# Optimization experiments

Hardware: AMD Instinct MI355X
Metric: run time of the kernel (lower is better)

Reference implementation:

```python
import jax, jax.numpy as jnp
import numpy as np

B, T, E, HEAD_S = 8, 4096, 2048, 128


def setup_inputs() -> dict:
    key = jax.random.key(0)
    kx, kq, kk, kv = jax.random.split(key, 4)
    x = jax.random.normal(kx, (B, T, E), dtype=jnp.float32)
    # Linear weights initialized ~N(0, 0.02) as in the repo's _init_weights
    Wq = jax.random.normal(kq, (E, HEAD_S), dtype=jnp.float32) * 0.02
    Wk = jax.random.normal(kk, (E, HEAD_S), dtype=jnp.float32) * 0.02
    Wv = jax.random.normal(kv, (E, HEAD_S), dtype=jnp.float32) * 0.02
    return {"x": x, "Wq": Wq, "Wk": Wk, "Wv": Wv}


def reference(x, Wq, Wk, Wv):
    # x: [B,T,E]; W*: [E,D]
    q = jnp.einsum('bte,ed->btd', x, Wq)
    k = jnp.einsum('bte,ed->btd', x, Wk)
    v = jnp.einsum('bte,ed->btd', x, Wv)
    scale = k.shape[-1] ** -0.5
    # scores: [B, T(query), S(key)]
    wei = jnp.einsum('btd,bsd->bts', q, k) * scale
    Tn = x.shape[1]
    causal = jnp.tril(jnp.ones((Tn, Tn), dtype=bool))  # [T,S], True where allowed
    wei = jnp.where(causal[None, :, :], wei, -jnp.inf)
    # NOTE: original code applies softmax over dim=1 (the QUERY axis) —
    # faithful reproduction of that behavior. Each key-column j has finite
    # entries for queries i >= j, so no NaNs arise.
    wei = jax.nn.softmax(wei, axis=1)
    # dropout is identity in eval mode
    out = jnp.einsum('bts,bsd->btd', wei, v)  # [B,T,D]
    return out
```

## Files before the change

kernel.cpp:

```cpp
#include <hip/hip_runtime.h>
#include <hip/hip_bf16.h>

#define TLEN 4096
#define EDIM 2048
#define DDIM 128
#define BSZ  8
#define NT   32
#define MROWS (BSZ*TLEN)
#define NSLOT 528

typedef unsigned short u16;
typedef __attribute__((ext_vector_type(8))) short bf16x8;
typedef __attribute__((ext_vector_type(4))) float f32x4;

#define C1F (0.08838834764831845f * 1.4426950408889634f)

__device__ __forceinline__ u16 f2bf(float f) {
  unsigned u = __builtin_bit_cast(unsigned, f);
  u += 0x7FFFu + ((u >> 16) & 1u);
  return (u16)(u >> 16);
}
__device__ __forceinline__ float bf2f(u16 h) {
  unsigned u = ((unsigned)h) << 16;
  return __builtin_bit_cast(float, u);
}

__device__ __forceinline__ void async_ld16(const void* g, void* lds) {
  __builtin_amdgcn_global_load_lds(
      (const __attribute__((address_space(1))) unsigned int*)(g),
      (__attribute__((address_space(3))) unsigned int*)(lds), 16, 0, 0);
}

__device__ __forceinline__ int swz16(int row, int chunk) {
  return row * 256 + ((chunk ^ (row & 15)) << 4);
}
__device__ __forceinline__ int swz8(int row, int chunk) {
  return row * 128 + ((chunk ^ (row & 7)) << 4);
}

__global__ __launch_bounds__(256) void zero_f32(float* __restrict__ out,
                                                float* __restrict__ denom) {
  size_t i = (size_t)blockIdx.x * 256 + threadIdx.x;
  float4 z = {0.f, 0.f, 0.f, 0.f};
  if (i < (size_t)MROWS * DDIM / 4) ((float4*)out)[i] = z;
  if (i < (size_t)BSZ * TLEN / 4) ((float4*)denom)[i] = z;
}

__global__ __launch_bounds__(256) void prep_w(const float* __restrict__ Wq,
                                              const float* __restrict__ Wk,
                                              const float* __restrict__ Wv,
                                              u16* __restrict__ Wt) {
  int g = blockIdx.x * 256 + threadIdx.x;
  int w = g >> 15;
  int rem = g & 32767;
  int n = rem >> 8;
  int k0 = (rem & 255) * 8;
  const float* W = (w == 0) ? Wq : (w == 1) ? Wk : Wv;
  unsigned pk[4];
  for (int i = 0; i < 4; ++i) {
    u16 lo = f2bf(W[(size_t)(k0 + 2 * i) * DDIM + n]);
    u16 hi = f2bf(W[(size_t)(k0 + 2 * i + 1) * DDIM + n]);
    pk[i] = (unsigned)lo | ((unsigned)hi << 16);
  }
  uint4 v; v.x = pk[0]; v.y = pk[1]; v.z = pk[2]; v.w = pk[3];
  *(uint4*)(Wt + ((size_t)(w * DDIM + n) * EDIM + k0)) = v;
}

__global__ __launch_bounds__(512, 2) void qkv_gemm(const float* __restrict__ x,
                                                   const u16* __restrict__ Wt,
                                                   u16* __restrict__ qkvb) {
  __shared__ u16 As[128 * 64];
  __shared__ u16 Bs[384 * 64];
  const int tid = threadIdx.x, lane = tid & 63, wave = tid >> 6;
  const int quad = lane >> 4, l15 = lane & 15;
  const int m0 = blockIdx.x * 128;
  const int wm = wave & 1, wn = wave >> 1;

  const f32x4 zero = {0.f, 0.f, 0.f, 0.f};
  f32x4 acc[4][6];
  for (int mi = 0; mi < 4; ++mi)
    for (int ni = 0; ni < 6; ++ni) acc[mi][ni] = zero;

  int arow[4], af4[4];
  for (int i = 0; i < 4; ++i) {
    int c = i * 512 + tid;
    arow[i] = c >> 4;
    af4[i] = c & 15;
  }
  float4 ap[4];
#define LOADA(KT)                                                            \
  for (int i = 0; i < 4; ++i)                                                \
    ap[i] = *(const float4*)(x + (size_t)(m0 + arow[i]) * EDIM + (KT)*64 +   \
                             af4[i] * 4);
  LOADA(0)

  for (int kt = 0; kt < EDIM / 64; ++kt) {
    __syncthreads();
    for (int i = 0; i < 4; ++i) {
      uint2 pk;
      pk.x = (unsigned)f2bf(ap[i].x) | ((unsigned)f2bf(ap[i].y) << 16);
      pk.y = (unsigned)f2bf(ap[i].z) | ((unsigned)f2bf(ap[i].w) << 16);
      *(uint2*)((char*)As + swz8(arow[i], af4[i] >> 1) + (af4[i] & 1) * 8) = pk;
    }
    {
      const int k0 = kt * 64;
      for (int e = 0; e < 6; ++e) {
        int rb = (wave * 6 + e) * 8;
        int r = rb + (lane >> 3);
        int c = (lane & 7) ^ (r & 7);
        async_ld16((const char*)(Wt + (size_t)r * EDIM + k0) + c * 16,
                   (char*)Bs + rb * 128);
      }
    }
    __builtin_amdgcn_s_waitcnt(0);
    __syncthreads();
    if (kt + 1 < EDIM / 64) { LOADA(kt + 1) }
    for (int ks = 0; ks < 2; ++ks) {
      const int ch = ks * 4 + quad;
      bf16x8 afr[4], bfr[6];
      for (int mi = 0; mi < 4; ++mi)
        afr[mi] = *(const bf16x8*)((char*)As + swz8(wm * 64 + mi * 16 + l15, ch));
      for (int ni = 0; ni < 6; ++ni)
        bfr[ni] = *(const bf16x8*)((char*)Bs + swz8(wn * 96 + ni * 16 + l15, ch));
      for (int mi = 0; mi < 4; ++mi)
        for (int ni = 0; ni < 6; ++ni)
          acc[mi][ni] = __builtin_amdgcn_mfma_f32_16x16x32_bf16(afr[mi], bfr[ni], acc[mi][ni], 0, 0, 0);
    }
  }
#undef LOADA
  for (int mi = 0; mi < 4; ++mi)
    for (int ni = 0; ni < 6; ++ni) {
      int n = wn * 96 + ni * 16 + l15;
      u16* ob = qkvb + (size_t)(n >> 7) * MROWS * DDIM;
      int nc = n & 127;
      for (int r = 0; r < 4; ++r) {
        int row = m0 + wm * 64 + mi * 16 + quad * 4 + r;
        ob[(size_t)row * DDIM + nc] = f2bf(acc[mi][ni][r]);
      }
    }
}

__global__ __launch_bounds__(256) void score_k(const u16* __restrict__ qb,
                                               const u16* __restrict__ kb,
                                               char* __restrict__ Epack,
                                               float* __restrict__ denom) {
  __shared__ u16 Kbuf[128 * 128];
  __shared__ u16 Qbuf[128 * 128];
  const int tid = threadIdx.x, lane = tid & 63, wave = tid >> 6;
  const int quad = lane >> 4, l15 = lane & 15;
  const int jt = blockIdx.x, ic = blockIdx.y, b = blockIdx.z;
  const int len = NT - jt;
  const int cl = (len + 3) >> 2;
  if (ic * cl >= len) return;
  const int beg = jt + ic * cl;
  const int end = (beg + cl < NT) ? beg + cl : NT;
  const int j0 = jt * 128;

  {
    const char* gk = (const char*)kb + (size_t)(b * TLEN + j0) * 256;
    for (int e = 0; e < 8; ++e) {
      int rb = (wave * 8 + e) * 4;
      int r = rb + (lane >> 4);
      int c = l15 ^ (r & 15);
      async_ld16(gk + r * 256 + c * 16, (char*)Kbuf + rb * 256);
    }
  }
  __builtin_amdgcn_s_waitcnt(0);
  __syncthreads();

  float csum[8];
  for (int ni = 0; ni < 8; ++ni) csum[ni] = 0.f;
  const f32x4 zero = {0.f, 0.f, 0.f, 0.f};

  for (int it = beg; it < end; ++it) {
    const int i0 = it * 128;
    {
      const char* gq = (const char*)qb + (size_t)(b * TLEN + i0) * 256;
      for (int e = 0; e < 8; ++e) {
        int rb = (wave * 8 + e) * 4;
        int r = rb + (lane >> 4);
        int c = l15 ^ (r & 15);
        async_ld16(gq + r * 256 + c * 16, (char*)Qbuf + rb * 256);
      }
    }
    __builtin_amdgcn_s_waitcnt(0);

    f32x4 accS[2][8];
    for (int mi = 0; mi < 2; ++mi)
      for (int ni = 0; ni < 8; ++ni) accS[mi][ni] = zero;
    for (int ks = 0; ks < 4; ++ks) {
      const int ch = ks * 4 + quad;
      bf16x8 afr[2], kfr[8];
      for (int mi = 0; mi < 2; ++mi)
        afr[mi] = *(const bf16x8*)((char*)Qbuf + swz16(wave * 32 + mi * 16 + l15, ch));
      for (int ni = 0; ni < 8; ++ni)
        kfr[ni] = *(const bf16x8*)((char*)Kbuf + swz16(ni * 16 + l15, ch));
      for (int mi = 0; mi < 2; ++mi)
        for (int ni = 0; ni < 8; ++ni)
          accS[mi][ni] = __builtin_amdgcn_mfma_f32_16x16x32_bf16(afr[mi], kfr[ni], accS[mi][ni], 0, 0, 0);
    }
    const bool diag = (it == jt);
    for (int mi = 0; mi < 2; ++mi)
      for (int ni = 0; ni < 8; ++ni)
        for (int r = 0; r < 4; ++r) {
          float e = exp2f(C1F * accS[mi][ni][r]);
          int rrow = wave * 32 + mi * 16 + quad * 4 + r;
          int jl = ni * 16 + l15;
          if (diag && (i0 + rrow) < (j0 + jl)) e = 0.f;
          csum[ni] += e;
          *(u16*)((char*)Qbuf + swz16(rrow, jl >> 3) + (jl & 7) * 2) = f2bf(e);
        }
    char* eslot = Epack + (((size_t)b * NSLOT + (size_t)it * (it + 1) / 2 + jt) << 15);
    for (int e = 0; e < 8; ++e) {
      int row = wave * 32 + e * 4 + (lane >> 4);
      bf16x8 v = *(const bf16x8*)((char*)Qbuf + swz16(row, l15));
      *(bf16x8*)(eslot + row * 256 + l15 * 16) = v;
    }
  }
  for (int ni = 0; ni < 8; ++ni) {
    csum[ni] += __shfl_xor(csum[ni], 16, 64);
    csum[ni] += __shfl_xor(csum[ni], 32, 64);
  }
  __syncthreads();
  float* red = (float*)Kbuf;
  if (lane < 16)
    for (int ni = 0; ni < 8; ++ni)
      red[wave * 128 + ni * 16 + lane] = csum[ni];
  __syncthreads();
  if (tid < 128)
    atomicAdd(&denom[(size_t)b * TLEN + j0 + tid],
              red[tid] + red[128 + tid] + red[256 + tid] + red[384 + tid]);
}

__global__ __launch_bounds__(256) void vscale_t(const u16* __restrict__ vb,
                                                const float* __restrict__ denom,
                                                u16* __restrict__ vbT) {
  __shared__ u16 tile[128 * 136];
  const int tid = threadIdx.x;
  const int t0 = blockIdx.x * 128, b = blockIdx.y;
  for (int i = 0; i < 8; ++i) {
    int c = tid + i * 256;
    int tl = c >> 4, ch = c & 15;
    float rd = 1.0f / denom[(size_t)b * TLEN + t0 + tl];
    uint4 v = *(const uint4*)(vb + ((size_t)(b * TLEN + t0 + tl) * DDIM + ch * 8));
    unsigned w[4] = {v.x, v.y, v.z, v.w};
    unsigned o[4];
    for (int j = 0; j < 4; ++j) {
      float lo = bf2f((u16)w[j]) * rd;
      float hi = bf2f((u16)(w[j] >> 16)) * rd;
      o[j] = (unsigned)f2bf(lo) | ((unsigned)f2bf(hi) << 16);
    }
    uint4 ov; ov.x = o[0]; ov.y = o[1]; ov.z = o[2]; ov.w = o[3];
    *(uint4*)(tile + tl * 136 + ch * 8) = ov;
  }
  __syncthreads();
  for (int i = 0; i < 8; ++i) {
    int c = tid + i * 256;
    int d = c >> 4, ch = c & 15;
    unsigned pk[4];
    for (int j = 0; j < 4; ++j) {
      u16 lo = tile[(ch * 8 + 2 * j) * 136 + d];
      u16 hi = tile[(ch * 8 + 2 * j + 1) * 136 + d];
      pk[j] = (unsigned)lo | ((unsigned)hi << 16);
    }
    uint4 v; v.x = pk[0]; v.y = pk[1]; v.z = pk[2]; v.w = pk[3];
    *(uint4*)(vbT + ((size_t)(b * DDIM + d) * TLEN + t0 + ch * 8)) = v;
  }
}

__global__ __launch_bounds__(256, 3) void pv_k(const char* __restrict__ Epack,
                                               const u16* __restrict__ vbT,
                                               float* __restrict__ out) {
  __shared__ u16 Es[128 * 64];
  __shared__ u16 Vs[128 * 64];
  const int tid = threadIdx.x, lane = tid & 63, wave = tid >> 6;
  const int quad = lane >> 4, l15 = lane & 15;
  const int it = blockIdx.x, jc = blockIdx.y, b = blockIdx.z;
  const int nsub = 2 * (it + 1);
  const int sBeg = jc * 16;
  if (sBeg >= nsub) return;
  const int sEnd = (sBeg + 16 < nsub) ? sBeg + 16 : nsub;
  const int i0 = it * 128;
  const int wm = wave & 1, wn = wave >> 1;

  const f32x4 zero = {0.f, 0.f, 0.f, 0.f};
  f32x4 accO[4][4];
  for (int mi = 0; mi < 4; ++mi)
    for (int ni = 0; ni < 4; ++ni) accO[mi][ni] = zero;

  const size_t triBase = ((size_t)b * NSLOT + (size_t)it * (it + 1) / 2) << 15;
  const char* vbase = (const char*)vbT + (size_t)b * DDIM * TLEN * 2;

  for (int s = sBeg; s < sEnd; ++s) {
    const int jt = s >> 1, h = s & 1;
    __syncthreads();
    {
      const char* eb = Epack + triBase + ((size_t)jt << 15) + h * 128;
      const char* vb2 = vbase + s * 128;
      for (int e = 0; e < 4; ++e) {
        int rb = (wave * 4 + e) * 8;
        int r = rb + (lane >> 3);
        int c = (lane & 7) ^ (r & 7);
        async_ld16(eb + r * 256 + c * 16, (char*)Es + rb * 128);
        async_ld16(vb2 + (size_t)r * (TLEN * 2) + c * 16, (char*)Vs + rb * 128);
      }
    }
    __builtin_amdgcn_s_waitcnt(0);
    __syncthreads();
    for (int ks = 0; ks < 2; ++ks) {
      const int ch = ks * 4 + quad;
      bf16x8 afr[4], bfr[4];
      for (int mi = 0; mi < 4; ++mi)
        afr[mi] = *(const bf16x8*)((char*)Es + swz8(wm * 64 + mi * 16 + l15, ch));
      for (int ni = 0; ni < 4; ++ni)
        bfr[ni] = *(const bf16x8*)((char*)Vs + swz8(wn * 64 + ni * 16 + l15, ch));
      for (int mi = 0; mi < 4; ++mi)
        for (int ni = 0; ni < 4; ++ni)
          accO[mi][ni] = __builtin_amdgcn_mfma_f32_16x16x32_bf16(afr[mi], bfr[ni], accO[mi][ni], 0, 0, 0);
    }
  }
  const bool excl = (it < 8);
  for (int mi = 0; mi < 4; ++mi)
    for (int ni = 0; ni < 4; ++ni) {
      int d = wn * 64 + ni * 16 + l15;
      for (int r = 0; r < 4; ++r) {
        int row = i0 + wm * 64 + mi * 16 + quad * 4 + r;
        float* dst = &out[((size_t)b * TLEN + row) * DDIM + d];
        if (excl) *dst = accO[mi][ni][r];
        else atomicAdd(dst, accO[mi][ni][r]);
      }
    }
}

extern "C" void kernel_launch(void* const* d_in, const int* in_sizes, int n_in,
                              void* d_out, int out_size, void* d_ws, size_t ws_size,
                              hipStream_t stream) {
  const float* x  = (const float*)d_in[0];
  const float* Wq = (const float*)d_in[1];
  const float* Wk = (const float*)d_in[2];
  const float* Wv = (const float*)d_in[3];
  float* out = (float*)d_out;

  u16* qb  = (u16*)d_ws;
  u16* kb  = qb  + (size_t)MROWS * DDIM;
  u16* vb  = kb  + (size_t)MROWS * DDIM;
  u16* vbT = vb  + (size_t)MROWS * DDIM;
  u16* Wt  = vbT + (size_t)MROWS * DDIM;
  float* denom = (float*)(Wt + (size_t)3 * DDIM * EDIM);
  char* Epack = (char*)(denom + (size_t)BSZ * TLEN);

  hipLaunchKernelGGL(zero_f32, dim3(4096), dim3(256), 0, stream, out, denom);
  hipLaunchKernelGGL(prep_w, dim3(384), dim3(256), 0, stream, Wq, Wk, Wv, Wt);
  hipLaunchKernelGGL(qkv_gemm, dim3(256), dim3(512), 0, stream, x, Wt, qb);
  hipLaunchKernelGGL(score_k, dim3(NT, 4, BSZ), dim3(256), 0, stream, qb, kb, Epack, denom);
  hipLaunchKernelGGL(vscale_t, dim3(NT, BSZ), dim3(256), 0, stream, vb, denom, vbT);
  hipLaunchKernelGGL(pv_k, dim3(NT, 4, BSZ), dim3(256), 0, stream, Epack, vbT, out);
}
```

Measured before the change: 623.5 us.

## Drop LDS staging in score and PV kernels, load operands directly from global

score_k now swaps operand roles (K as A, Q as B) so the exponentials can be packed and written straight to the E slab without an LDS transpose, and reads Q fragments directly from global memory instead of staging them in shared memory. The column-sum reduction moves to 16-lane shuffles. pv_k drops its LDS tiles and barriers, reads E and V fragments directly from global, walks full 128-wide key tiles, reverses block order so the largest rows start first, and halves the key split (excl threshold adjusted). Launch bounds also change for qkv_gemm and score_k. The trade is fewer barriers and LDS traffic against uncoalesced or repeated global loads that rely on cache hits.

```diff
diff --git a/kernel.cpp b/kernel.cpp
--- a/kernel.cpp
+++ b/kernel.cpp
@@ -66,7 +66,7 @@
   *(uint4*)(Wt + ((size_t)(w * DDIM + n) * EDIM + k0)) = v;
 }
 
-__global__ __launch_bounds__(512, 2) void qkv_gemm(const float* __restrict__ x,
+__global__ __launch_bounds__(512, 1) void qkv_gemm(const float* __restrict__ x,
                                                    const u16* __restrict__ Wt,
                                                    u16* __restrict__ qkvb) {
   __shared__ u16 As[128 * 64];
@@ -140,12 +140,12 @@
     }
 }
 
-__global__ __launch_bounds__(256) void score_k(const u16* __restrict__ qb,
-                                               const u16* __restrict__ kb,
-                                               char* __restrict__ Epack,
-                                               float* __restrict__ denom) {
+__global__ __launch_bounds__(256, 2) void score_k(const u16* __restrict__ qb,
+                                                  const u16* __restrict__ kb,
+                                                  char* __restrict__ Epack,
+                                                  float* __restrict__ denom) {
   __shared__ u16 Kbuf[128 * 128];
-  __shared__ u16 Qbuf[128 * 128];
+  __shared__ float red[512];
   const int tid = threadIdx.x, lane = tid & 63, wave = tid >> 6;
   const int quad = lane >> 4, l15 = lane & 15;
   const int jt = blockIdx.x, ic = blockIdx.y, b = blockIdx.z;
@@ -157,7 +157,7 @@
   const int j0 = jt * 128;
 
   {
-    const char* gk = (const char*)kb + (size_t)(b * TLEN + j0) * 256;
+    const char* gk = (const char*)kb + ((size_t)b * TLEN + j0) * 256;
     for (int e = 0; e < 8; ++e) {
       int rb = (wave * 8 + e) * 4;
       int r = rb + (lane >> 4);
@@ -168,64 +168,62 @@
   __builtin_amdgcn_s_waitcnt(0);
   __syncthreads();
 
-  float csum[8];
-  for (int ni = 0; ni < 8; ++ni) csum[ni] = 0.f;
+  float csum[8][4];
+  for (int mi = 0; mi < 8; ++mi)
+    for (int r = 0; r < 4; ++r) csum[mi][r] = 0.f;
   const f32x4 zero = {0.f, 0.f, 0.f, 0.f};
+  const char* qtile0 = (const char*)qb + (size_t)b * TLEN * 256;
 
   for (int it = beg; it < end; ++it) {
     const int i0 = it * 128;
-    {
-      const char* gq = (const char*)qb + (size_t)(b * TLEN + i0) * 256;
-      for (int e = 0; e < 8; ++e) {
-        int rb = (wave * 8 + e) * 4;
-        int r = rb + (lane >> 4);
-        int c = l15 ^ (r & 15);
-        async_ld16(gq + r * 256 + c * 16, (char*)Qbuf + rb * 256);
-      }
-    }
-    __builtin_amdgcn_s_waitcnt(0);
-
-    f32x4 accS[2][8];
-    for (int mi = 0; mi < 2; ++mi)
-      for (int ni = 0; ni < 8; ++ni) accS[mi][ni] = zero;
+    const char* gq = qtile0 + (size_t)i0 * 256;
+    f32x4 acc[8][2];
+    for (int mi = 0; mi < 8; ++mi)
+      for (int ni = 0; ni < 2; ++ni) acc[mi][ni] = zero;
     for (int ks = 0; ks < 4; ++ks) {
       const int ch = ks * 4 + quad;
-      bf16x8 afr[2], kfr[8];
-      for (int mi = 0; mi < 2; ++mi)
-        afr[mi] = *(const bf16x8*)((char*)Qbuf + swz16(wave * 32 + mi * 16 + l15, ch));
-      for (int ni = 0; ni < 8; ++ni)
-        kfr[ni] = *(const bf16x8*)((char*)Kbuf + swz16(ni * 16 + l15, ch));
-      for (int mi = 0; mi < 2; ++mi)
-        for (int ni = 0; ni < 8; ++ni)
-          accS[mi][ni] = __builtin_amdgcn_mfma_f32_16x16x32_bf16(afr[mi], kfr[ni], accS[mi][ni], 0, 0, 0);
+      bf16x8 kfr[8], qfr[2];
+      for (int ni = 0; ni < 2; ++ni)
+        qfr[ni] = *(const bf16x8*)(gq + (size_t)(wave * 32 + ni * 16 + l15) * 256 + ch * 16);
+      for (int mi = 0; mi < 8; ++mi)
+        kfr[mi] = *(const bf16x8*)((char*)Kbuf + swz16(mi * 16 + l15, ch));
+      for (int mi = 0; mi < 8; ++mi)
+        for (int ni = 0; ni < 2; ++ni)
+          acc[mi][ni] = __builtin_amdgcn_mfma_f32_16x16x32_bf16(kfr[mi], qfr[ni], acc[mi][ni], 0, 0, 0);
     }
     const bool diag = (it == jt);
-    for (int mi = 0; mi < 2; ++mi)
-      for (int ni = 0; ni < 8; ++ni)
+    char* eslot = Epack + (((size_t)b * NSLOT + (size_t)it * (it + 1) / 2 + jt) << 15);
+    for (int mi = 0; mi < 8; ++mi) {
+      const int jbase = mi * 16 + quad * 4;
+      for (int ni = 0; ni < 2; ++ni) {
+        const int il = wave * 32 + ni * 16 + l15;
+        float ev[4];
         for (int r = 0; r < 4; ++r) {
-          float e = exp2f(C1F * accS[mi][ni][r]);
-          int rrow = wave * 32 + mi * 16 + quad * 4 + r;
-          int jl = ni * 16 + l15;
-          if (diag && (i0 + rrow) < (j0 + jl)) e = 0.f;
-          csum[ni] += e;
-          *(u16*)((char*)Qbuf + swz16(rrow, jl >> 3) + (jl & 7) * 2) = f2bf(e);
+          float e = __builtin_amdgcn_exp2f(C1F * acc[mi][ni][r]);
+          if (diag && (i0 + il) < (j0 + jbase + r)) e = 0.f;
+          csum[mi][r] += e;
+          ev[r] = e;
         }
-    char* eslot = Epack + (((size_t)b * NSLOT + (size_t)it * (it + 1) / 2 + jt) << 15);
-    for (int e = 0; e < 8; ++e) {
-      int row = wave * 32 + e * 4 + (lane >> 4);
-      bf16x8 v = *(const bf16x8*)((char*)Qbuf + swz16(row, l15));
-      *(bf16x8*)(eslot + row * 256 + l15 * 16) = v;
-    }
-  }
-  for (int ni = 0; ni < 8; ++ni) {
-    csum[ni] += __shfl_xor(csum[ni], 16, 64);
-    csum[ni] += __shfl_xor(csum[ni], 32, 64);
-  }
-  __syncthreads();
-  float* red = (float*)Kbuf;
-  if (lane < 16)
-    for (int ni = 0; ni < 8; ++ni)
-      red[wave * 128 + ni * 16 + lane] = csum[ni];
+        uint2 pk;
+        pk.x = (unsigned)f2bf(ev[0]) | ((unsigned)f2bf(ev[1]) << 16);
+        pk.y = (unsigned)f2bf(ev[2]) | ((unsigned)f2bf(ev[3]) << 16);
+        *(uint2*)(eslot + (size_t)il * 256 + jbase * 2) = pk;
+      }
+    }
+  }
+  for (int mi = 0; mi < 8; ++mi)
+    for (int r = 0; r < 4; ++r) {
+      float v = csum[mi][r];
+      v += __shfl_xor(v, 1, 64);
+      v += __shfl_xor(v, 2, 64);
+      v += __shfl_xor(v, 4, 64);
+      v += __shfl_xor(v, 8, 64);
+      csum[mi][r] = v;
+    }
+  if (l15 == 0)
+    for (int mi = 0; mi < 8; ++mi)
+      for (int r = 0; r < 4; ++r)
+        red[wave * 128 + mi * 16 + quad * 4 + r] = csum[mi][r];
   __syncthreads();
   if (tid < 128)
     atomicAdd(&denom[(size_t)b * TLEN + j0 + tid],
@@ -271,15 +269,12 @@
 __global__ __launch_bounds__(256, 3) void pv_k(const char* __restrict__ Epack,
                                                const u16* __restrict__ vbT,
                                                float* __restrict__ out) {
-  __shared__ u16 Es[128 * 64];
-  __shared__ u16 Vs[128 * 64];
   const int tid = threadIdx.x, lane = tid & 63, wave = tid >> 6;
   const int quad = lane >> 4, l15 = lane & 15;
-  const int it = blockIdx.x, jc = blockIdx.y, b = blockIdx.z;
-  const int nsub = 2 * (it + 1);
-  const int sBeg = jc * 16;
-  if (sBeg >= nsub) return;
-  const int sEnd = (sBeg + 16 < nsub) ? sBeg + 16 : nsub;
+  const int it = NT - 1 - blockIdx.x, jc = blockIdx.y, b = blockIdx.z;
+  const int jtBeg = jc * 16;
+  if (jtBeg > it) return;
+  const int jtEnd = (jtBeg + 16 < it + 1) ? jtBeg + 16 : it + 1;
   const int i0 = it * 128;
   const int wm = wave & 1, wn = wave >> 1;
 
@@ -288,38 +283,25 @@
   for (int mi = 0; mi < 4; ++mi)
     for (int ni = 0; ni < 4; ++ni) accO[mi][ni] = zero;
 
-  const size_t triBase = ((size_t)b * NSLOT + (size_t)it * (it + 1) / 2) << 15;
+  const char* triBase = Epack + (((size_t)b * NSLOT + (size_t)it * (it + 1) / 2) << 15);
   const char* vbase = (const char*)vbT + (size_t)b * DDIM * TLEN * 2;
 
-  for (int s = sBeg; s < sEnd; ++s) {
-    const int jt = s >> 1, h = s & 1;
-    __syncthreads();
-    {
-      const char* eb = Epack + triBase + ((size_t)jt << 15) + h * 128;
-      const char* vb2 = vbase + s * 128;
-      for (int e = 0; e < 4; ++e) {
-        int rb = (wave * 4 + e) * 8;
-        int r = rb + (lane >> 3);
-        int c = (lane & 7) ^ (r & 7);
-        async_ld16(eb + r * 256 + c * 16, (char*)Es + rb * 128);
-        async_ld16(vb2 + (size_t)r * (TLEN * 2) + c * 16, (char*)Vs + rb * 128);
-      }
-    }
-    __builtin_amdgcn_s_waitcnt(0);
-    __syncthreads();
-    for (int ks = 0; ks < 2; ++ks) {
-      const int ch = ks * 4 + quad;
+  for (int jt = jtBeg; jt < jtEnd; ++jt) {
+    const char* eb = triBase + ((size_t)jt << 15);
+    const char* vb2 = vbase + jt * 256;
+    for (int ks = 0; ks < 4; ++ks) {
+      const int choff = (ks * 4 + quad) * 16;
       bf16x8 afr[4], bfr[4];
       for (int mi = 0; mi < 4; ++mi)
-        afr[mi] = *(const bf16x8*)((char*)Es + swz8(wm * 64 + mi * 16 + l15, ch));
+        afr[mi] = *(const bf16x8*)(eb + (size_t)(wm * 64 + mi * 16 + l15) * 256 + choff);
       for (int ni = 0; ni < 4; ++ni)
-        bfr[ni] = *(const bf16x8*)((char*)Vs + swz8(wn * 64 + ni * 16 + l15, ch));
+        bfr[ni] = *(const bf16x8*)(vb2 + (size_t)(wn * 64 + ni * 16 + l15) * (TLEN * 2) + choff);
       for (int mi = 0; mi < 4; ++mi)
         for (int ni = 0; ni < 4; ++ni)
           accO[mi][ni] = __builtin_amdgcn_mfma_f32_16x16x32_bf16(afr[mi], bfr[ni], accO[mi][ni], 0, 0, 0);
     }
   }
-  const bool excl = (it < 8);
+  const bool excl = (it < 16);
   for (int mi = 0; mi < 4; ++mi)
     for (int ni = 0; ni < 4; ++ni) {
       int d = wn * 64 + ni * 16 + l15;
@@ -354,5 +336,5 @@
   hipLaunchKernelGGL(qkv_gemm, dim3(256), dim3(512), 0, stream, x, Wt, qb);
   hipLaunchKernelGGL(score_k, dim3(NT, 4, BSZ), dim3(256), 0, stream, qb, kb, Epack, denom);
   hipLaunchKernelGGL(vscale_t, dim3(NT, BSZ), dim3(256), 0, stream, vb, denom, vbT);
-  hipLaunchKernelGGL(pv_k, dim3(NT, 4, BSZ), dim3(256), 0, stream, Epack, vbT, out);
-}
+  hipLaunchKernelGGL(pv_k, dim3(NT, 2, BSZ), dim3(256), 0, stream, Epack, vbT, out);
+}
```

New measurement: 705.2 us. 13.1% more time.
